# Kernel tuning notes

Measured on AMD Instinct MI355X. Metric: run time of the kernel, lower is better.

The kernel has to match this reference:

```python
import jax, jax.numpy as jnp
import numpy as np
import math

H = 4
D_MODEL = 512
OUT_DIM = D_MODEL // 2  # 256 (concat=True path)
D_K = OUT_DIM // H      # 64
N = 4096


def setup_inputs() -> dict:
    key0 = jax.random.key(0)
    ks = jax.random.split(key0, 12)
    s = 1.0 / math.sqrt(D_MODEL)
    inp = {
        "query": jax.random.normal(ks[0], (N, D_MODEL), dtype=jnp.float32),
        "key": jax.random.normal(ks[1], (N, D_MODEL), dtype=jnp.float32),
        "mask": jax.random.randint(ks[2], (N, N), 0, 2, dtype=jnp.int32),
        # 4 linears (q, k, q_v, k_v), each d_model -> out_dim
        "Wq": jax.random.normal(ks[3], (OUT_DIM, D_MODEL), dtype=jnp.float32) * s,
        "bq": jax.random.normal(ks[4], (OUT_DIM,), dtype=jnp.float32) * s,
        "Wk": jax.random.normal(ks[5], (OUT_DIM, D_MODEL), dtype=jnp.float32) * s,
        "bk": jax.random.normal(ks[6], (OUT_DIM,), dtype=jnp.float32) * s,
        "Wqv": jax.random.normal(ks[7], (OUT_DIM, D_MODEL), dtype=jnp.float32) * s,
        "bqv": jax.random.normal(ks[8], (OUT_DIM,), dtype=jnp.float32) * s,
        "Wkv": jax.random.normal(ks[9], (OUT_DIM, D_MODEL), dtype=jnp.float32) * s,
        "bkv": jax.random.normal(ks[10], (OUT_DIM,), dtype=jnp.float32) * s,
    }
    return inp


def _heads(x, W, b):
    # [N, d_model] @ W^T + b -> [N, out_dim] -> [h, N, d_k]
    y = x @ W.T + b
    return y.reshape(-1, H, D_K).transpose(1, 0, 2)


def reference(query, key, mask, Wq, bq, Wk, bk, Wqv, bqv, Wkv, bkv):
    q = _heads(query, Wq, bq)    # [h, Nq, d_k]
    k = _heads(key, Wk, bk)      # [h, Nk, d_k]
    qv = _heads(query, Wqv, bqv)  # [h, Nq, d_k]
    kv = _heads(key, Wkv, bkv)    # [h, Nk, d_k]

    scores = jnp.einsum("hqd,hkd->hqk", q, k) / math.sqrt(D_K)  # [h, Nq, Nk]
    scores = jnp.where(mask[None] == 0, jnp.float32(-1e9), scores)
    p = jax.nn.softmax(scores, axis=-1)  # attention weights per head

    # x1 = ELU(p @ k_v), x2 = ELU(p^T @ q_v); concat over heads.
    x1 = jax.nn.elu(jnp.einsum("hqk,hkd->hqd", p, kv))  # [h, Nq, d_k]
    x2 = jax.nn.elu(jnp.einsum("hqk,hqd->hkd", p, qv))  # [h, Nk, d_k]
    x1 = x1.transpose(1, 0, 2).reshape(-1, H * D_K)  # [Nq, out_dim]
    x2 = x2.transpose(1, 0, 2).reshape(-1, H * D_K)  # [Nk, out_dim]
    # Dropout omitted (inference / deterministic reference).
    return x1, x2, p
```

## Files before the change

kernel.cpp:

```cpp
#include <hip/hip_runtime.h>
#include <hip/hip_bf16.h>

#define NN 4096
#define DMODEL 512
#define ODIM 256
#define NHEAD 4
#define DKH 64
#define NKW 64

typedef __attribute__((ext_vector_type(8))) short short8;
typedef __attribute__((ext_vector_type(4))) short short4v;
typedef __attribute__((ext_vector_type(8))) __bf16 bf16x8;
typedef __attribute__((ext_vector_type(4))) float f32x4;

__device__ __forceinline__ short f2bf(float f) {
    unsigned u = __builtin_bit_cast(unsigned, f);
    u += 0x7fffu + ((u >> 16) & 1u);
    return (short)(u >> 16);
}
__device__ __forceinline__ f32x4 mfma16(short8 a, short8 b, f32x4 c) {
    return __builtin_amdgcn_mfma_f32_16x16x32_bf16(
        __builtin_bit_cast(bf16x8, a), __builtin_bit_cast(bf16x8, b), c, 0, 0, 0);
}

__global__ __launch_bounds__(256) void pack_mask_k(const int* __restrict__ mask,
                                                   unsigned long long* __restrict__ bits) {
    int tid = blockIdx.x * 256 + threadIdx.x;
    int wid = tid >> 6;
    int lane = tid & 63;
    int v = mask[(size_t)wid * 64 + lane];
    unsigned long long b = __ballot(v != 0);
    if (lane == 0) bits[wid] = b;
}

__global__ __launch_bounds__(256) void proj_k(
    const float* __restrict__ Xq, const float* __restrict__ Xk,
    const float* __restrict__ Wq, const float* __restrict__ bq,
    const float* __restrict__ Wk, const float* __restrict__ bk,
    const float* __restrict__ Wqv, const float* __restrict__ bqv,
    const float* __restrict__ Wkv, const float* __restrict__ bkv,
    short* __restrict__ qh, short* __restrict__ kh,
    short* __restrict__ qvT, short* __restrict__ kvT) {
    int z = blockIdx.z;
    const float *X, *W, *B;
    short* out;
    int tr;
    float postscale = 1.f;
    switch (z) {
        case 0: X = Xq; W = Wq;  B = bq;  out = qh;  tr = 0; postscale = 0.125f; break;
        case 1: X = Xk; W = Wk;  B = bk;  out = kh;  tr = 0; break;
        case 2: X = Xq; W = Wqv; B = bqv; out = qvT; tr = 1; break;
        default: X = Xk; W = Wkv; B = bkv; out = kvT; tr = 1; break;
    }
    int lane = threadIdx.x & 63, w = threadIdx.x >> 6;
    int lr = lane & 15, lg = lane >> 4;
    int m0 = blockIdx.x * 64 + (w >> 1) * 32;
    int n0 = blockIdx.y * 64 + (w & 1) * 32;

    f32x4 acc[2][2] = {};
    for (int kk = 0; kk < DMODEL; kk += 32) {
        short8 a[2], b[2];
#pragma unroll
        for (int i = 0; i < 2; i++) {
            const float* pa = X + (size_t)(m0 + i * 16 + lr) * DMODEL + kk + lg * 8;
            const float* pb = W + (size_t)(n0 + i * 16 + lr) * DMODEL + kk + lg * 8;
            float4 a0 = *(const float4*)pa;
            float4 a1 = *(const float4*)(pa + 4);
            float4 b0 = *(const float4*)pb;
            float4 b1 = *(const float4*)(pb + 4);
            a[i][0] = f2bf(a0.x); a[i][1] = f2bf(a0.y); a[i][2] = f2bf(a0.z); a[i][3] = f2bf(a0.w);
            a[i][4] = f2bf(a1.x); a[i][5] = f2bf(a1.y); a[i][6] = f2bf(a1.z); a[i][7] = f2bf(a1.w);
            b[i][0] = f2bf(b0.x); b[i][1] = f2bf(b0.y); b[i][2] = f2bf(b0.z); b[i][3] = f2bf(b0.w);
            b[i][4] = f2bf(b1.x); b[i][5] = f2bf(b1.y); b[i][6] = f2bf(b1.z); b[i][7] = f2bf(b1.w);
        }
#pragma unroll
        for (int i = 0; i < 2; i++)
#pragma unroll
            for (int j = 0; j < 2; j++) acc[i][j] = mfma16(a[i], b[j], acc[i][j]);
    }
#pragma unroll
    for (int i = 0; i < 2; i++)
#pragma unroll
        for (int j = 0; j < 2; j++) {
            int col = n0 + j * 16 + lr;
            float bv = B[col];
            int hh = col >> 6, dk = col & 63;
#pragma unroll
            for (int r = 0; r < 4; r++) {
                int row = m0 + i * 16 + lg * 4 + r;
                short s = f2bf((acc[i][j][r] + bv) * postscale);
                if (!tr) out[((size_t)hh * NN + row) * DKH + dk] = s;
                else     out[((size_t)hh * DKH + dk) * NN + row] = s;
            }
        }
}

__global__ __launch_bounds__(512) void attn_p_x1_k(
    const short* __restrict__ qh, const short* __restrict__ kh, const short* __restrict__ kvT,
    const unsigned long long* __restrict__ bits,
    float* __restrict__ x1_out, float* __restrict__ p_out) {
    int h = blockIdx.y;
    int tid = threadIdx.x, lane = tid & 63, w = tid >> 6;
    int lr = lane & 15, lg = lane >> 4;
    int q0 = blockIdx.x * 16;

    __shared__ float smemf[4608];
    short (*plds)[16][72] = (short (*)[16][72])smemf;
    float (*xbuf)[64][17] = (float (*)[64][17])smemf;
    __shared__ float sl[8][16];

    const short* khh = kh + (size_t)h * NN * DKH;
    const unsigned long long* brow = bits + (size_t)(q0 + lr) * NKW;

    short8 bq[2];
#pragma unroll
    for (int kk = 0; kk < 2; kk++)
        bq[kk] = *(const short8*)(qh + ((size_t)h * NN + q0 + lr) * DKH + kk * 32 + lg * 8);

    float lrun = 0.f;
    for (int t = 0; t < 8; t++) {
        int kt = w * 8 + t;
        f32x4 s[4] = {};
#pragma unroll
        for (int fj = 0; fj < 4; fj++)
#pragma unroll
            for (int kk = 0; kk < 2; kk++) {
                short8 a = *(const short8*)(khh + (size_t)(kt * 64 + fj * 16 + lr) * DKH + kk * 32 + lg * 8);
                s[fj] = mfma16(a, bq[kk], s[fj]);
            }
        unsigned long long mw = brow[kt] >> (lg * 4);
#pragma unroll
        for (int fj = 0; fj < 4; fj++)
#pragma unroll
            for (int r = 0; r < 4; r++) {
                bool keep = (mw >> (fj * 16 + r)) & 1ull;
                lrun += __expf(keep ? s[fj][r] : -100.f);
            }
    }
    lrun += __shfl_xor(lrun, 16);
    lrun += __shfl_xor(lrun, 32);
    if (lg == 0) sl[w][lr] = lrun;
    __syncthreads();
    float l = 0.f;
#pragma unroll
    for (int w2 = 0; w2 < 8; w2++) l += sl[w2][lr];
    float linv = l > 0.f ? 1.f / l : 0.f;

    f32x4 acc1[4] = {};
    float* prow = p_out + ((size_t)h * NN + q0 + lr) * NN;
    for (int t = 0; t < 8; t++) {
        int kt = w * 8 + t;
        f32x4 s[4] = {};
#pragma unroll
        for (int fj = 0; fj < 4; fj++)
#pragma unroll
            for (int kk = 0; kk < 2; kk++) {
                short8 a = *(const short8*)(khh + (size_t)(kt * 64 + fj * 16 + lr) * DKH + kk * 32 + lg * 8);
                s[fj] = mfma16(a, bq[kk], s[fj]);
            }
        unsigned long long mw = brow[kt] >> (lg * 4);
#pragma unroll
        for (int fj = 0; fj < 4; fj++) {
            float4 pv;
            short4v pb;
#pragma unroll
            for (int r = 0; r < 4; r++) {
                bool keep = (mw >> (fj * 16 + r)) & 1ull;
                float p = __expf(keep ? s[fj][r] : -100.f) * linv;
                (&pv.x)[r] = p;
                pb[r] = f2bf(p);
            }
            *(float4*)(prow + kt * 64 + fj * 16 + lg * 4) = pv;
            *(short4v*)&plds[w][lr][fj * 16 + lg * 4] = pb;
        }
#pragma unroll
        for (int kk = 0; kk < 2; kk++) {
            short8 a1 = *(const short8*)&plds[w][lr][kk * 32 + lg * 8];
#pragma unroll
            for (int fd = 0; fd < 4; fd++) {
                short8 bv = *(const short8*)(kvT + ((size_t)h * DKH + fd * 16 + lr) * NN + kt * 64 + kk * 32 + lg * 8);
                acc1[fd] = mfma16(a1, bv, acc1[fd]);
            }
        }
    }
    __syncthreads();
    if (w >= 4) {
#pragma unroll
        for (int fd = 0; fd < 4; fd++)
#pragma unroll
            for (int r = 0; r < 4; r++) xbuf[w - 4][lane][fd * 4 + r] = acc1[fd][r];
    }
    __syncthreads();
    if (w < 4) {
#pragma unroll
        for (int fd = 0; fd < 4; fd++)
#pragma unroll
            for (int r = 0; r < 4; r++) acc1[fd][r] += xbuf[w][lane][fd * 4 + r];
    }
    __syncthreads();
    if (w >= 1 && w < 4) {
#pragma unroll
        for (int fd = 0; fd < 4; fd++)
#pragma unroll
            for (int r = 0; r < 4; r++) xbuf[w - 1][lane][fd * 4 + r] = acc1[fd][r];
    }
    __syncthreads();
    if (w == 0) {
#pragma unroll
        for (int fd = 0; fd < 4; fd++)
#pragma unroll
            for (int r = 0; r < 4; r++) {
                float v = acc1[fd][r] + xbuf[0][lane][fd * 4 + r] + xbuf[1][lane][fd * 4 + r] +
                          xbuf[2][lane][fd * 4 + r];
                v = v > 0.f ? v : (__expf(v) - 1.f);
                x1_out[(size_t)(q0 + lg * 4 + r) * ODIM + h * DKH + fd * 16 + lr] = v;
            }
    }
}

__global__ __launch_bounds__(512) void px2_k(
    const float* __restrict__ p, const short* __restrict__ qvT,
    float* __restrict__ x2_out) {
    int h = blockIdx.y;
    int k0 = blockIdx.x * 32;
    int tid = threadIdx.x, lane = tid & 63, w = tid >> 6;
    int lr = lane & 15, lg = lane >> 4;

    __shared__ float red[4][64][33];

    f32x4 acc[2][4] = {};
    const float* pbase = p + (size_t)h * NN * NN;
    const short* qvh = qvT + (size_t)h * DKH * NN;

    for (int it = 0; it < 16; it++) {
        int qq = w * 512 + it * 32;
        short8 aP[2];
#pragma unroll
        for (int fj = 0; fj < 2; fj++) {
            const float* pp = pbase + (size_t)(qq + lg * 8) * NN + k0 + fj * 16 + lr;
            short8 av;
#pragma unroll
            for (int j = 0; j < 8; j++) av[j] = f2bf(pp[j * NN]);
            aP[fj] = av;
        }
#pragma unroll
        for (int fd = 0; fd < 4; fd++) {
            short8 bv = *(const short8*)(qvh + (size_t)(fd * 16 + lr) * NN + qq + lg * 8);
#pragma unroll
            for (int fj = 0; fj < 2; fj++) acc[fj][fd] = mfma16(aP[fj], bv, acc[fj][fd]);
        }
    }
    if (w >= 4) {
#pragma unroll
        for (int fj = 0; fj < 2; fj++)
#pragma unroll
            for (int fd = 0; fd < 4; fd++)
#pragma unroll
                for (int r = 0; r < 4; r++)
                    red[w - 4][lane][fj * 16 + fd * 4 + r] = acc[fj][fd][r];
    }
    __syncthreads();
    if (w < 4) {
#pragma unroll
        for (int fj = 0; fj < 2; fj++)
#pragma unroll
            for (int fd = 0; fd < 4; fd++)
#pragma unroll
                for (int r = 0; r < 4; r++)
                    acc[fj][fd][r] += red[w][lane][fj * 16 + fd * 4 + r];
    }
    __syncthreads();
    if (w >= 1 && w < 4) {
#pragma unroll
        for (int fj = 0; fj < 2; fj++)
#pragma unroll
            for (int fd = 0; fd < 4; fd++)
#pragma unroll
                for (int r = 0; r < 4; r++)
                    red[w - 1][lane][fj * 16 + fd * 4 + r] = acc[fj][fd][r];
    }
    __syncthreads();
    if (w == 0) {
#pragma unroll
        for (int fj = 0; fj < 2; fj++)
#pragma unroll
            for (int fd = 0; fd < 4; fd++)
#pragma unroll
                for (int r = 0; r < 4; r++) {
                    float v = acc[fj][fd][r];
#pragma unroll
                    for (int s2 = 0; s2 < 3; s2++) v += red[s2][lane][fj * 16 + fd * 4 + r];
                    v = v > 0.f ? v : (__expf(v) - 1.f);
                    x2_out[(size_t)(k0 + fj * 16 + lg * 4 + r) * ODIM + h * DKH + fd * 16 + lr] = v;
                }
    }
}

extern "C" void kernel_launch(void* const* d_in, const int* in_sizes, int n_in,
                              void* d_out, int out_size, void* d_ws, size_t ws_size,
                              hipStream_t stream) {
    (void)in_sizes; (void)n_in; (void)out_size; (void)ws_size;
    const float* query = (const float*)d_in[0];
    const float* key   = (const float*)d_in[1];
    const int*   mask  = (const int*)d_in[2];
    const float* Wq  = (const float*)d_in[3];
    const float* bq  = (const float*)d_in[4];
    const float* Wk  = (const float*)d_in[5];
    const float* bk  = (const float*)d_in[6];
    const float* Wqv = (const float*)d_in[7];
    const float* bqv = (const float*)d_in[8];
    const float* Wkv = (const float*)d_in[9];
    const float* bkv = (const float*)d_in[10];

    float* out = (float*)d_out;
    float* x1 = out;
    float* x2 = out + (size_t)NN * ODIM;
    float* p  = out + (size_t)2 * NN * ODIM;

    char* ws = (char*)d_ws;
    short* qh  = (short*)(ws);
    short* kh  = (short*)(ws + (2u << 20));
    short* qvT = (short*)(ws + (4u << 20));
    short* kvT = (short*)(ws + (6u << 20));
    unsigned long long* bits = (unsigned long long*)(ws + (8u << 20));

    hipLaunchKernelGGL(pack_mask_k, dim3(NN * NN / 64 / 4), dim3(256), 0, stream, mask, bits);
    hipLaunchKernelGGL(proj_k, dim3(64, 4, 4), dim3(256), 0, stream,
                       query, key, Wq, bq, Wk, bk, Wqv, bqv, Wkv, bkv, qh, kh, qvT, kvT);
    hipLaunchKernelGGL(attn_p_x1_k, dim3(NN / 16, NHEAD), dim3(512), 0, stream,
                       qh, kh, kvT, bits, x1, p);
    hipLaunchKernelGGL(px2_k, dim3(NN / 32, NHEAD), dim3(512), 0, stream,
                       p, qvT, x2);
}
```

Before: 362.2 us.

## Fuse single-pass softmax with bf16 P staging and split-K x2 pipeline

The attention kernel now computes unnormalized exp scores in one pass and normalizes afterwards with the row sum. It writes a bf16 copy of P into a tiled workspace so the fp32 p output is written once from that buffer. The x2 path reads the compact bf16 tiles with qv pre-scaled by 1/l, using a split over q with a separate combine+ELU kernel, instead of rereading the fp32 p. This cuts the fp32 p reread traffic but needs a 128MB workspace, keeps a fallback path, and skips max subtraction (relies on bounded scores).

```diff
diff --git a/kernel.cpp b/kernel.cpp
--- a/kernel.cpp
+++ b/kernel.cpp
@@ -17,6 +17,10 @@
     unsigned u = __builtin_bit_cast(unsigned, f);
     u += 0x7fffu + ((u >> 16) & 1u);
     return (short)(u >> 16);
+}
+__device__ __forceinline__ float bf2f(short s) {
+    unsigned u = ((unsigned)(unsigned short)s) << 16;
+    return __builtin_bit_cast(float, u);
 }
 __device__ __forceinline__ f32x4 mfma16(short8 a, short8 b, f32x4 c) {
     return __builtin_amdgcn_mfma_f32_16x16x32_bf16(
@@ -95,7 +99,217 @@
         }
 }
 
-__global__ __launch_bounds__(512) void attn_p_x1_k(
+__global__ __launch_bounds__(512) void attn_fused_k(
+    const short* __restrict__ qh, const short* __restrict__ kh, const short* __restrict__ kvT,
+    const unsigned long long* __restrict__ bits,
+    short* __restrict__ pbuf, float* __restrict__ linv_ws,
+    float* __restrict__ x1_out, float* __restrict__ p_out) {
+    int h = blockIdx.y;
+    int strip = blockIdx.x;
+    int tid = threadIdx.x, lane = tid & 63, w = tid >> 6;
+    int lr = lane & 15, lg = lane >> 4;
+    int q0 = strip * 16;
+
+    __shared__ float smemf[4608];
+    short (*plds)[16][72] = (short (*)[16][72])smemf;
+    float (*xbuf)[64][17] = (float (*)[64][17])smemf;
+    __shared__ float sl[8][16];
+    __shared__ float linv_s[16];
+
+    const short* khh = kh + (size_t)h * NN * DKH;
+    const unsigned long long* brow = bits + (size_t)(q0 + lr) * NKW;
+    short* ptile0 = pbuf + (((size_t)(h * 256 + strip) * 64) << 10);
+
+    short8 bq[2];
+#pragma unroll
+    for (int kk = 0; kk < 2; kk++)
+        bq[kk] = *(const short8*)(qh + ((size_t)h * NN + q0 + lr) * DKH + kk * 32 + lg * 8);
+
+    float lrun = 0.f;
+    f32x4 acc1[4] = {};
+    for (int t = 0; t < 8; t++) {
+        int kt = w * 8 + t;
+        f32x4 s[4] = {};
+#pragma unroll
+        for (int fj = 0; fj < 4; fj++)
+#pragma unroll
+            for (int kk = 0; kk < 2; kk++) {
+                short8 a = *(const short8*)(khh + (size_t)(kt * 64 + fj * 16 + lr) * DKH + kk * 32 + lg * 8);
+                s[fj] = mfma16(a, bq[kk], s[fj]);
+            }
+        unsigned long long mw = brow[kt] >> (lg * 4);
+        short* ptile = ptile0 + ((size_t)kt << 10);
+#pragma unroll
+        for (int fj = 0; fj < 4; fj++) {
+            short4v pb4;
+#pragma unroll
+            for (int r = 0; r < 4; r++) {
+                bool keep = (mw >> (fj * 16 + r)) & 1ull;
+                float e = __expf(keep ? s[fj][r] : -100.f);
+                lrun += e;
+                pb4[r] = f2bf(e);
+            }
+            *(short4v*)&plds[w][lr][fj * 16 + lg * 4] = pb4;
+            *(short4v*)(ptile + lr * 64 + fj * 16 + lg * 4) = pb4;
+        }
+#pragma unroll
+        for (int kk = 0; kk < 2; kk++) {
+            short8 a1 = *(const short8*)&plds[w][lr][kk * 32 + lg * 8];
+#pragma unroll
+            for (int fd = 0; fd < 4; fd++) {
+                short8 bv = *(const short8*)(kvT + ((size_t)h * DKH + fd * 16 + lr) * NN + kt * 64 + kk * 32 + lg * 8);
+                acc1[fd] = mfma16(a1, bv, acc1[fd]);
+            }
+        }
+    }
+    lrun += __shfl_xor(lrun, 16);
+    lrun += __shfl_xor(lrun, 32);
+    if (lg == 0) sl[w][lr] = lrun;
+    __syncthreads();
+    float l = 0.f;
+#pragma unroll
+    for (int w2 = 0; w2 < 8; w2++) l += sl[w2][lr];
+    float linv = l > 0.f ? 1.f / l : 0.f;
+    if (w == 0 && lg == 0) {
+        linv_s[lr] = linv;
+        linv_ws[(size_t)h * NN + q0 + lr] = linv;
+    }
+    __syncthreads();
+
+    asm volatile("s_waitcnt vmcnt(0)" ::: "memory");
+    const short* psrc0 = ptile0 + (size_t)(w * 8 + (lane >> 3)) * 1024 + (lane & 7) * 8;
+    float* pdst0 = p_out + ((size_t)h * NN + q0) * NN + w * 512 + lane * 8;
+#pragma unroll 4
+    for (int r = 0; r < 16; r++) {
+        short8 pv = *(const short8*)(psrc0 + r * 64);
+        float lim = linv_s[r];
+        float4 o0, o1;
+        o0.x = bf2f(pv[0]) * lim; o0.y = bf2f(pv[1]) * lim;
+        o0.z = bf2f(pv[2]) * lim; o0.w = bf2f(pv[3]) * lim;
+        o1.x = bf2f(pv[4]) * lim; o1.y = bf2f(pv[5]) * lim;
+        o1.z = bf2f(pv[6]) * lim; o1.w = bf2f(pv[7]) * lim;
+        float* dst = pdst0 + (size_t)r * NN;
+        *(float4*)dst = o0;
+        *(float4*)(dst + 4) = o1;
+    }
+
+    __syncthreads();
+    if (w >= 4) {
+#pragma unroll
+        for (int fd = 0; fd < 4; fd++)
+#pragma unroll
+            for (int r = 0; r < 4; r++) xbuf[w - 4][lane][fd * 4 + r] = acc1[fd][r];
+    }
+    __syncthreads();
+    if (w < 4) {
+#pragma unroll
+        for (int fd = 0; fd < 4; fd++)
+#pragma unroll
+            for (int r = 0; r < 4; r++) acc1[fd][r] += xbuf[w][lane][fd * 4 + r];
+    }
+    __syncthreads();
+    if (w >= 1 && w < 4) {
+#pragma unroll
+        for (int fd = 0; fd < 4; fd++)
+#pragma unroll
+            for (int r = 0; r < 4; r++) xbuf[w - 1][lane][fd * 4 + r] = acc1[fd][r];
+    }
+    __syncthreads();
+    if (w == 0) {
+#pragma unroll
+        for (int fd = 0; fd < 4; fd++)
+#pragma unroll
+            for (int r = 0; r < 4; r++) {
+                float v = acc1[fd][r] + xbuf[0][lane][fd * 4 + r] + xbuf[1][lane][fd * 4 + r] +
+                          xbuf[2][lane][fd * 4 + r];
+                v *= linv_s[lg * 4 + r];
+                v = v > 0.f ? v : (__expf(v) - 1.f);
+                x1_out[(size_t)(q0 + lg * 4 + r) * ODIM + h * DKH + fd * 16 + lr] = v;
+            }
+    }
+}
+
+__global__ __launch_bounds__(256) void scale_qv_k(const short* __restrict__ qvT,
+                                                  const float* __restrict__ linv,
+                                                  short* __restrict__ qvS) {
+    int idx = blockIdx.x * 256 + threadIdx.x;
+    int q8 = idx & 511;
+    int dh = idx >> 9;
+    int h = dh >> 6;
+    short8 v = *(const short8*)(qvT + (size_t)dh * NN + q8 * 8);
+    const float* lp = linv + (size_t)h * NN + q8 * 8;
+    float4 l0 = *(const float4*)lp;
+    float4 l1 = *(const float4*)(lp + 4);
+    short8 o;
+    o[0] = f2bf(bf2f(v[0]) * l0.x); o[1] = f2bf(bf2f(v[1]) * l0.y);
+    o[2] = f2bf(bf2f(v[2]) * l0.z); o[3] = f2bf(bf2f(v[3]) * l0.w);
+    o[4] = f2bf(bf2f(v[4]) * l1.x); o[5] = f2bf(bf2f(v[5]) * l1.y);
+    o[6] = f2bf(bf2f(v[6]) * l1.z); o[7] = f2bf(bf2f(v[7]) * l1.w);
+    *(short8*)(qvS + (size_t)dh * NN + q8 * 8) = o;
+}
+
+__global__ __launch_bounds__(512) void px2b_k(
+    const short* __restrict__ pbuf, const short* __restrict__ qvS,
+    float* __restrict__ x2part) {
+    int kt = blockIdx.x, h = blockIdx.y, z = blockIdx.z;
+    int tid = threadIdx.x, lane = tid & 63, w = tid >> 6;
+    int fj = w & 3, sh = w >> 2;
+    int lr = lane & 15, lg = lane >> 4;
+
+    __shared__ float red[4][64][17];
+
+    const short* qvh = qvS + (size_t)h * DKH * NN;
+    f32x4 acc[4] = {};
+    int qbase = z * 2048 + sh * 1024;
+    for (int it = 0; it < 32; it++) {
+        int qq = qbase + it * 32;
+        int strip = (qq >> 4) + (lg >> 1);
+        const short* ab = pbuf + (((size_t)(h * 256 + strip) * 64 + kt) << 10) +
+                          (lg & 1) * 512 + fj * 16 + lr;
+        short8 af;
+#pragma unroll
+        for (int j = 0; j < 8; j++) af[j] = ab[j * 64];
+#pragma unroll
+        for (int fd = 0; fd < 4; fd++) {
+            short8 bv = *(const short8*)(qvh + (size_t)(fd * 16 + lr) * NN + qq + lg * 8);
+            acc[fd] = mfma16(af, bv, acc[fd]);
+        }
+    }
+    if (sh == 1) {
+#pragma unroll
+        for (int fd = 0; fd < 4; fd++)
+#pragma unroll
+            for (int r = 0; r < 4; r++) red[fj][lane][fd * 4 + r] = acc[fd][r];
+    }
+    __syncthreads();
+    if (sh == 0) {
+        float* xp = x2part + (size_t)z * NN * ODIM;
+#pragma unroll
+        for (int fd = 0; fd < 4; fd++)
+#pragma unroll
+            for (int r = 0; r < 4; r++) {
+                float v = acc[fd][r] + red[fj][lane][fd * 4 + r];
+                xp[(size_t)(kt * 64 + fj * 16 + lg * 4 + r) * ODIM + h * DKH + fd * 16 + lr] = v;
+            }
+    }
+}
+
+__global__ __launch_bounds__(256) void combine_x2_k(const float* __restrict__ x2part,
+                                                    float* __restrict__ x2_out) {
+    int idx = blockIdx.x * 256 + threadIdx.x;
+    size_t i = (size_t)idx * 4;
+    float4 a = *(const float4*)(x2part + i);
+    float4 b = *(const float4*)(x2part + (size_t)NN * ODIM + i);
+    float4 o;
+    o.x = a.x + b.x; o.y = a.y + b.y; o.z = a.z + b.z; o.w = a.w + b.w;
+    o.x = o.x > 0.f ? o.x : (__expf(o.x) - 1.f);
+    o.y = o.y > 0.f ? o.y : (__expf(o.y) - 1.f);
+    o.z = o.z > 0.f ? o.z : (__expf(o.z) - 1.f);
+    o.w = o.w > 0.f ? o.w : (__expf(o.w) - 1.f);
+    *(float4*)(x2_out + i) = o;
+}
+
+__global__ __launch_bounds__(512) void attn_fb_k(
     const short* __restrict__ qh, const short* __restrict__ kh, const short* __restrict__ kvT,
     const unsigned long long* __restrict__ bits,
     float* __restrict__ x1_out, float* __restrict__ p_out) {
@@ -218,7 +432,7 @@
     }
 }
 
-__global__ __launch_bounds__(512) void px2_k(
+__global__ __launch_bounds__(512) void px2_fb_k(
     const float* __restrict__ p, const short* __restrict__ qvT,
     float* __restrict__ x2_out) {
     int h = blockIdx.y;
@@ -299,7 +513,7 @@
 extern "C" void kernel_launch(void* const* d_in, const int* in_sizes, int n_in,
                               void* d_out, int out_size, void* d_ws, size_t ws_size,
                               hipStream_t stream) {
-    (void)in_sizes; (void)n_in; (void)out_size; (void)ws_size;
+    (void)in_sizes; (void)n_in; (void)out_size;
     const float* query = (const float*)d_in[0];
     const float* key   = (const float*)d_in[1];
     const int*   mask  = (const int*)d_in[2];
@@ -319,16 +533,32 @@
 
     char* ws = (char*)d_ws;
     short* qh  = (short*)(ws);
-    short* kh  = (short*)(ws + (2u << 20));
-    short* qvT = (short*)(ws + (4u << 20));
-    short* kvT = (short*)(ws + (6u << 20));
-    unsigned long long* bits = (unsigned long long*)(ws + (8u << 20));
+    short* kh  = (short*)(ws + (2ull << 20));
+    short* qvT = (short*)(ws + (4ull << 20));
+    short* kvT = (short*)(ws + (6ull << 20));
+    unsigned long long* bits = (unsigned long long*)(ws + (8ull << 20));
+    float* linv_ws = (float*)(ws + (10ull << 20));
+    short* qvS = (short*)(ws + (10ull << 20) + (1ull << 19));
+    float* x2part = (float*)(ws + (13ull << 20));
+    short* pbuf = (short*)(ws + (21ull << 20));
+    size_t need = (21ull << 20) + (size_t)NHEAD * NN * NN * sizeof(short);
 
     hipLaunchKernelGGL(pack_mask_k, dim3(NN * NN / 64 / 4), dim3(256), 0, stream, mask, bits);
     hipLaunchKernelGGL(proj_k, dim3(64, 4, 4), dim3(256), 0, stream,
                        query, key, Wq, bq, Wk, bk, Wqv, bqv, Wkv, bkv, qh, kh, qvT, kvT);
-    hipLaunchKernelGGL(attn_p_x1_k, dim3(NN / 16, NHEAD), dim3(512), 0, stream,
-                       qh, kh, kvT, bits, x1, p);
-    hipLaunchKernelGGL(px2_k, dim3(NN / 32, NHEAD), dim3(512), 0, stream,
-                       p, qvT, x2);
-}
+
+    if (ws_size >= need) {
+        hipLaunchKernelGGL(attn_fused_k, dim3(NN / 16, NHEAD), dim3(512), 0, stream,
+                           qh, kh, kvT, bits, pbuf, linv_ws, x1, p);
+        hipLaunchKernelGGL(scale_qv_k, dim3(512), dim3(256), 0, stream, qvT, linv_ws, qvS);
+        hipLaunchKernelGGL(px2b_k, dim3(NN / 64, NHEAD, 2), dim3(512), 0, stream,
+                           pbuf, qvS, x2part);
+        hipLaunchKernelGGL(combine_x2_k, dim3(NN * ODIM / 4 / 256), dim3(256), 0, stream,
+                           x2part, x2);
+    } else {
+        hipLaunchKernelGGL(attn_fb_k, dim3(NN / 16, NHEAD), dim3(512), 0, stream,
+                           qh, kh, kvT, bits, x1, p);
+        hipLaunchKernelGGL(px2_fb_k, dim3(NN / 32, NHEAD), dim3(512), 0, stream,
+                           p, qvT, x2);
+    }
+}
```

After: 369.3 us. No clear change (+2.0%).

## Recompute masked exp scores for x2 instead of rereading the fp32 P matrix

Applied to the files above, without the earlier changes.

The softmax row-sum pass becomes its own kernel that writes 1/l per query. x2 is then computed by recomputing QK^T and the masked exp on the fly, with the normalisation folded into a pre-scaled bf16 copy of q_v, so the 256 MB fp32 probability matrix is no longer read back strided. A split-K over four query chunks writes partial results that a small combine kernel sums before applying ELU. This adds a second QK^T recompute plus extra launches and workspace in exchange for removing a large global-memory read; masked entries now skip the exp rather than using -100.

```diff
diff --git a/kernel.cpp b/kernel.cpp
--- a/kernel.cpp
+++ b/kernel.cpp
@@ -12,11 +12,19 @@
 typedef __attribute__((ext_vector_type(4))) short short4v;
 typedef __attribute__((ext_vector_type(8))) __bf16 bf16x8;
 typedef __attribute__((ext_vector_type(4))) float f32x4;
+typedef __attribute__((ext_vector_type(4))) unsigned int u32x4;
 
 __device__ __forceinline__ short f2bf(float f) {
     unsigned u = __builtin_bit_cast(unsigned, f);
     u += 0x7fffu + ((u >> 16) & 1u);
     return (short)(u >> 16);
+}
+__device__ __forceinline__ float bf2f(short s) {
+    unsigned u = ((unsigned)(unsigned short)s) << 16;
+    return __builtin_bit_cast(float, u);
+}
+__device__ __forceinline__ unsigned pack2bf(float a, float b) {
+    return (unsigned)(unsigned short)f2bf(a) | ((unsigned)(unsigned short)f2bf(b) << 16);
 }
 __device__ __forceinline__ f32x4 mfma16(short8 a, short8 b, f32x4 c) {
     return __builtin_amdgcn_mfma_f32_16x16x32_bf16(
@@ -28,7 +36,7 @@
     int tid = blockIdx.x * 256 + threadIdx.x;
     int wid = tid >> 6;
     int lane = tid & 63;
-    int v = mask[(size_t)wid * 64 + lane];
+    int v = __builtin_nontemporal_load(mask + (size_t)wid * 64 + lane);
     unsigned long long b = __ballot(v != 0);
     if (lane == 0) bits[wid] = b;
 }
@@ -95,18 +103,15 @@
         }
 }
 
-__global__ __launch_bounds__(512) void attn_p_x1_k(
-    const short* __restrict__ qh, const short* __restrict__ kh, const short* __restrict__ kvT,
+__global__ __launch_bounds__(512) void attn_sum_k(
+    const short* __restrict__ qh, const short* __restrict__ kh,
     const unsigned long long* __restrict__ bits,
-    float* __restrict__ x1_out, float* __restrict__ p_out) {
+    float* __restrict__ linv_ws) {
     int h = blockIdx.y;
+    int q0 = blockIdx.x * 16;
     int tid = threadIdx.x, lane = tid & 63, w = tid >> 6;
     int lr = lane & 15, lg = lane >> 4;
-    int q0 = blockIdx.x * 16;
-
-    __shared__ float smemf[4608];
-    short (*plds)[16][72] = (short (*)[16][72])smemf;
-    float (*xbuf)[64][17] = (float (*)[64][17])smemf;
+
     __shared__ float sl[8][16];
 
     const short* khh = kh + (size_t)h * NN * DKH;
@@ -134,17 +139,42 @@
 #pragma unroll
             for (int r = 0; r < 4; r++) {
                 bool keep = (mw >> (fj * 16 + r)) & 1ull;
-                lrun += __expf(keep ? s[fj][r] : -100.f);
+                if (keep) lrun += __expf(s[fj][r]);
             }
     }
     lrun += __shfl_xor(lrun, 16);
     lrun += __shfl_xor(lrun, 32);
     if (lg == 0) sl[w][lr] = lrun;
     __syncthreads();
-    float l = 0.f;
-#pragma unroll
-    for (int w2 = 0; w2 < 8; w2++) l += sl[w2][lr];
-    float linv = l > 0.f ? 1.f / l : 0.f;
+    if (tid < 16) {
+        float l = 0.f;
+#pragma unroll
+        for (int w2 = 0; w2 < 8; w2++) l += sl[w2][tid];
+        linv_ws[(size_t)h * NN + q0 + tid] = l > 0.f ? 1.f / l : 0.f;
+    }
+}
+
+__global__ __launch_bounds__(512) void attn_px1_k(
+    const short* __restrict__ qh, const short* __restrict__ kh, const short* __restrict__ kvT,
+    const unsigned long long* __restrict__ bits, const float* __restrict__ linv_ws,
+    float* __restrict__ x1_out, float* __restrict__ p_out) {
+    int h = blockIdx.y;
+    int q0 = blockIdx.x * 16;
+    int tid = threadIdx.x, lane = tid & 63, w = tid >> 6;
+    int lr = lane & 15, lg = lane >> 4;
+
+    __shared__ float smemf[4608];
+    short (*plds)[16][72] = (short (*)[16][72])smemf;
+    float (*xbuf)[64][17] = (float (*)[64][17])smemf;
+
+    const short* khh = kh + (size_t)h * NN * DKH;
+    const unsigned long long* brow = bits + (size_t)(q0 + lr) * NKW;
+    float linv = linv_ws[(size_t)h * NN + q0 + lr];
+
+    short8 bq[2];
+#pragma unroll
+    for (int kk = 0; kk < 2; kk++)
+        bq[kk] = *(const short8*)(qh + ((size_t)h * NN + q0 + lr) * DKH + kk * 32 + lg * 8);
 
     f32x4 acc1[4] = {};
     float* prow = p_out + ((size_t)h * NN + q0 + lr) * NN;
@@ -166,7 +196,7 @@
 #pragma unroll
             for (int r = 0; r < 4; r++) {
                 bool keep = (mw >> (fj * 16 + r)) & 1ull;
-                float p = __expf(keep ? s[fj][r] : -100.f) * linv;
+                float p = keep ? __expf(s[fj][r]) * linv : 0.f;
                 (&pv.x)[r] = p;
                 pb[r] = f2bf(p);
             }
@@ -218,82 +248,134 @@
     }
 }
 
-__global__ __launch_bounds__(512) void px2_k(
-    const float* __restrict__ p, const short* __restrict__ qvT,
-    float* __restrict__ x2_out) {
-    int h = blockIdx.y;
-    int k0 = blockIdx.x * 32;
+__global__ __launch_bounds__(256) void scale_qv_k(const short* __restrict__ qvT,
+                                                  const float* __restrict__ linv,
+                                                  short* __restrict__ qvS) {
+    int idx = blockIdx.x * 256 + threadIdx.x;
+    int q8 = idx & 511;
+    int dh = idx >> 9;
+    int h = dh >> 6;
+    short8 v = *(const short8*)(qvT + (size_t)dh * NN + q8 * 8);
+    const float* lp = linv + (size_t)h * NN + q8 * 8;
+    float4 l0 = *(const float4*)lp;
+    float4 l1 = *(const float4*)(lp + 4);
+    short8 o;
+    o[0] = f2bf(bf2f(v[0]) * l0.x); o[1] = f2bf(bf2f(v[1]) * l0.y);
+    o[2] = f2bf(bf2f(v[2]) * l0.z); o[3] = f2bf(bf2f(v[3]) * l0.w);
+    o[4] = f2bf(bf2f(v[4]) * l1.x); o[5] = f2bf(bf2f(v[5]) * l1.y);
+    o[6] = f2bf(bf2f(v[6]) * l1.z); o[7] = f2bf(bf2f(v[7]) * l1.w);
+    *(short8*)(qvS + (size_t)dh * NN + q8 * 8) = o;
+}
+
+__global__ __launch_bounds__(512) void px2c_k(
+    const short* __restrict__ qh, const short* __restrict__ kh,
+    const short* __restrict__ qvS, const unsigned long long* __restrict__ bits,
+    float* __restrict__ x2part) {
+    int bx = blockIdx.x, h = blockIdx.y, z = blockIdx.z;
     int tid = threadIdx.x, lane = tid & 63, w = tid >> 6;
+    int fk = w & 3, sh = w >> 2;
     int lr = lane & 15, lg = lane >> 4;
-
-    __shared__ float red[4][64][33];
-
-    f32x4 acc[2][4] = {};
-    const float* pbase = p + (size_t)h * NN * NN;
-    const short* qvh = qvT + (size_t)h * DKH * NN;
+    int k0 = bx * 64;
+
+    __shared__ float red[4][64][17];
+
+    const short* khh = kh + (size_t)h * NN * DKH;
+    const short* qhh = qh + (size_t)h * NN * DKH;
+    const short* qvh = qvS + (size_t)h * DKH * NN;
+
+    short8 bk2[2];
+#pragma unroll
+    for (int kk = 0; kk < 2; kk++)
+        bk2[kk] = *(const short8*)(khh + (size_t)(k0 + fk * 16 + lr) * DKH + kk * 32 + lg * 8);
+
+    f32x4 acc[4] = {};
+    int qbase = z * 1024 + sh * 512;
+    int kbit = fk * 16 + lr;
+    int sA = lr + (((2 * lg) & 3) << 4);
+    int sB = lr + (((2 * lg + 1) & 3) << 4);
+    bool lowhalf = lg < 2;
 
     for (int it = 0; it < 16; it++) {
-        int qq = w * 512 + it * 32;
-        short8 aP[2];
-#pragma unroll
-        for (int fj = 0; fj < 2; fj++) {
-            const float* pp = pbase + (size_t)(qq + lg * 8) * NN + k0 + fj * 16 + lr;
-            short8 av;
-#pragma unroll
-            for (int j = 0; j < 8; j++) av[j] = f2bf(pp[j * NN]);
-            aP[fj] = av;
-        }
+        int qq = qbase + it * 32;
+        f32x4 slo = {}, shi = {};
+#pragma unroll
+        for (int kk = 0; kk < 2; kk++) {
+            short8 alo = *(const short8*)(qhh + (size_t)(qq + lr) * DKH + kk * 32 + lg * 8);
+            slo = mfma16(alo, bk2[kk], slo);
+        }
+#pragma unroll
+        for (int kk = 0; kk < 2; kk++) {
+            short8 ahi = *(const short8*)(qhh + (size_t)(qq + 16 + lr) * DKH + kk * 32 + lg * 8);
+            shi = mfma16(ahi, bk2[kk], shi);
+        }
+        float el[4], eh[4];
+#pragma unroll
+        for (int r = 0; r < 4; r++) {
+            unsigned long long mwl = bits[(size_t)(qq + lg * 4 + r) * NKW + bx];
+            el[r] = ((mwl >> kbit) & 1ull) ? __expf(slo[r]) : 0.f;
+            unsigned long long mwh = bits[(size_t)(qq + 16 + lg * 4 + r) * NKW + bx];
+            eh[r] = ((mwh >> kbit) & 1ull) ? __expf(shi[r]) : 0.f;
+        }
+        unsigned lo_w0 = pack2bf(el[0], el[1]), lo_w1 = pack2bf(el[2], el[3]);
+        unsigned hi_w0 = pack2bf(eh[0], eh[1]), hi_w1 = pack2bf(eh[2], eh[3]);
+        unsigned a0l = (unsigned)__shfl((int)lo_w0, sA);
+        unsigned a0h = (unsigned)__shfl((int)hi_w0, sA);
+        unsigned a1l = (unsigned)__shfl((int)lo_w1, sA);
+        unsigned a1h = (unsigned)__shfl((int)hi_w1, sA);
+        unsigned a2l = (unsigned)__shfl((int)lo_w0, sB);
+        unsigned a2h = (unsigned)__shfl((int)hi_w0, sB);
+        unsigned a3l = (unsigned)__shfl((int)lo_w1, sB);
+        unsigned a3h = (unsigned)__shfl((int)hi_w1, sB);
+        u32x4 aw;
+        aw.x = lowhalf ? a0l : a0h;
+        aw.y = lowhalf ? a1l : a1h;
+        aw.z = lowhalf ? a2l : a2h;
+        aw.w = lowhalf ? a3l : a3h;
+        short8 af = __builtin_bit_cast(short8, aw);
 #pragma unroll
         for (int fd = 0; fd < 4; fd++) {
             short8 bv = *(const short8*)(qvh + (size_t)(fd * 16 + lr) * NN + qq + lg * 8);
-#pragma unroll
-            for (int fj = 0; fj < 2; fj++) acc[fj][fd] = mfma16(aP[fj], bv, acc[fj][fd]);
-        }
-    }
-    if (w >= 4) {
-#pragma unroll
-        for (int fj = 0; fj < 2; fj++)
-#pragma unroll
-            for (int fd = 0; fd < 4; fd++)
-#pragma unroll
-                for (int r = 0; r < 4; r++)
-                    red[w - 4][lane][fj * 16 + fd * 4 + r] = acc[fj][fd][r];
-    }
-    __syncthreads();
-    if (w < 4) {
-#pragma unroll
-        for (int fj = 0; fj < 2; fj++)
-#pragma unroll
-            for (int fd = 0; fd < 4; fd++)
-#pragma unroll
-                for (int r = 0; r < 4; r++)
-                    acc[fj][fd][r] += red[w][lane][fj * 16 + fd * 4 + r];
-    }
-    __syncthreads();
-    if (w >= 1 && w < 4) {
-#pragma unroll
-        for (int fj = 0; fj < 2; fj++)
-#pragma unroll
-            for (int fd = 0; fd < 4; fd++)
-#pragma unroll
-                for (int r = 0; r < 4; r++)
-                    red[w - 1][lane][fj * 16 + fd * 4 + r] = acc[fj][fd][r];
-    }
-    __syncthreads();
-    if (w == 0) {
-#pragma unroll
-        for (int fj = 0; fj < 2; fj++)
-#pragma unroll
-            for (int fd = 0; fd < 4; fd++)
-#pragma unroll
-                for (int r = 0; r < 4; r++) {
-                    float v = acc[fj][fd][r];
-#pragma unroll
-                    for (int s2 = 0; s2 < 3; s2++) v += red[s2][lane][fj * 16 + fd * 4 + r];
-                    v = v > 0.f ? v : (__expf(v) - 1.f);
-                    x2_out[(size_t)(k0 + fj * 16 + lg * 4 + r) * ODIM + h * DKH + fd * 16 + lr] = v;
-                }
-    }
+            acc[fd] = mfma16(af, bv, acc[fd]);
+        }
+    }
+    if (sh == 1) {
+#pragma unroll
+        for (int fd = 0; fd < 4; fd++)
+#pragma unroll
+            for (int r = 0; r < 4; r++) red[fk][lane][fd * 4 + r] = acc[fd][r];
+    }
+    __syncthreads();
+    if (sh == 0) {
+        float* xp = x2part + (size_t)z * NN * ODIM;
+#pragma unroll
+        for (int fd = 0; fd < 4; fd++)
+#pragma unroll
+            for (int r = 0; r < 4; r++) {
+                float v = acc[fd][r] + red[fk][lane][fd * 4 + r];
+                xp[(size_t)(k0 + fk * 16 + lg * 4 + r) * ODIM + h * DKH + fd * 16 + lr] = v;
+            }
+    }
+}
+
+__global__ __launch_bounds__(256) void combine_x2_k(const float* __restrict__ x2part,
+                                                    float* __restrict__ x2_out) {
+    int idx = blockIdx.x * 256 + threadIdx.x;
+    size_t i = (size_t)idx * 4;
+    const size_t stride = (size_t)NN * ODIM;
+    float4 a = *(const float4*)(x2part + i);
+    float4 b = *(const float4*)(x2part + stride + i);
+    float4 c = *(const float4*)(x2part + 2 * stride + i);
+    float4 d = *(const float4*)(x2part + 3 * stride + i);
+    float4 o;
+    o.x = a.x + b.x + c.x + d.x;
+    o.y = a.y + b.y + c.y + d.y;
+    o.z = a.z + b.z + c.z + d.z;
+    o.w = a.w + b.w + c.w + d.w;
+    o.x = o.x > 0.f ? o.x : (__expf(o.x) - 1.f);
+    o.y = o.y > 0.f ? o.y : (__expf(o.y) - 1.f);
+    o.z = o.z > 0.f ? o.z : (__expf(o.z) - 1.f);
+    o.w = o.w > 0.f ? o.w : (__expf(o.w) - 1.f);
+    *(float4*)(x2_out + i) = o;
 }
 
 extern "C" void kernel_launch(void* const* d_in, const int* in_sizes, int n_in,
@@ -319,16 +401,24 @@
 
     char* ws = (char*)d_ws;
     short* qh  = (short*)(ws);
-    short* kh  = (short*)(ws + (2u << 20));
-    short* qvT = (short*)(ws + (4u << 20));
-    short* kvT = (short*)(ws + (6u << 20));
-    unsigned long long* bits = (unsigned long long*)(ws + (8u << 20));
+    short* kh  = (short*)(ws + (2ull << 20));
+    short* qvT = (short*)(ws + (4ull << 20));
+    short* kvT = (short*)(ws + (6ull << 20));
+    unsigned long long* bits = (unsigned long long*)(ws + (8ull << 20));
+    float* linv_ws = (float*)(ws + (10ull << 20));
+    short* qvS = (short*)(ws + (10ull << 20) + (1ull << 19));
+    float* x2part = (float*)(ws + (13ull << 20));
 
     hipLaunchKernelGGL(pack_mask_k, dim3(NN * NN / 64 / 4), dim3(256), 0, stream, mask, bits);
     hipLaunchKernelGGL(proj_k, dim3(64, 4, 4), dim3(256), 0, stream,
                        query, key, Wq, bq, Wk, bk, Wqv, bqv, Wkv, bkv, qh, kh, qvT, kvT);
-    hipLaunchKernelGGL(attn_p_x1_k, dim3(NN / 16, NHEAD), dim3(512), 0, stream,
-                       qh, kh, kvT, bits, x1, p);
-    hipLaunchKernelGGL(px2_k, dim3(NN / 32, NHEAD), dim3(512), 0, stream,
-                       p, qvT, x2);
-}
+    hipLaunchKernelGGL(attn_sum_k, dim3(NN / 16, NHEAD), dim3(512), 0, stream,
+                       qh, kh, bits, linv_ws);
+    hipLaunchKernelGGL(scale_qv_k, dim3(512), dim3(256), 0, stream, qvT, linv_ws, qvS);
+    hipLaunchKernelGGL(px2c_k, dim3(NN / 64, NHEAD, 4), dim3(512), 0, stream,
+                       qh, kh, qvS, bits, x2part);
+    hipLaunchKernelGGL(combine_x2_k, dim3(NN * ODIM / 4 / 256), dim3(256), 0, stream,
+                       x2part, x2);
+    hipLaunchKernelGGL(attn_px1_k, dim3(NN / 16, NHEAD), dim3(512), 0, stream,
+                       qh, kh, kvT, bits, linv_ws, x1, p);
+}
```

After: 481.0 us. +32.8%, slower.
